# Optimization experiments

Hardware: AMD Instinct MI355X
Metric: run time of the kernel (lower is better)

The kernel has to match this reference:

```python
import jax, jax.numpy as jnp
import numpy as np

B, S, D, H, C = 2, 2048, 1024, 16, 64

def setup_inputs() -> dict:
    key = jax.random.key(0)
    kx, kq, kk, kv, ko = jax.random.split(key, 5)
    scale = 0.02
    return {
        "x": jax.random.normal(kx, (B, S, D), dtype=jnp.float32),
        "Wq": jax.random.normal(kq, (D, H, C), dtype=jnp.float32) * scale,
        "Wk": jax.random.normal(kk, (D, H, C), dtype=jnp.float32) * scale,
        "Wv": jax.random.normal(kv, (D, H, C), dtype=jnp.float32) * scale,
        "Wo": jax.random.normal(ko, (H, C, D), dtype=jnp.float32) * scale,
    }

def reference(x, Wq, Wk, Wv, Wo):
    # project to per-head q/k/v: [B,S,H,C]
    q = jnp.einsum('bqd,dhc->bqhc', x, Wq)
    k = jnp.einsum('bkd,dhc->bkhc', x, Wk)
    v = jnp.einsum('bkd,dhc->bkhc', x, Wv)
    q = q * (C ** -0.5)
    alphas = jnp.einsum('bqhc,bkhc->bhqk', q, k)  # [B,H,S,S]
    weights = jax.nn.softmax(alphas, axis=-1)
    out = jnp.einsum('bhqk,bkhc->bqhc', weights, v)
    return jnp.einsum('bqhc,hcd->bqd', out, Wo)
```

## Files before the change

kernel.cpp:

```cpp
#include <hip/hip_runtime.h>
#include <hip/hip_bf16.h>
#include <stdint.h>
#include <stddef.h>

typedef __bf16 bf16;
typedef __bf16 bf16x8 __attribute__((ext_vector_type(8)));
typedef float f32x4 __attribute__((ext_vector_type(4)));

#define DEV __device__ __forceinline__

DEV void async16(const bf16* g, bf16* l) {
    __builtin_amdgcn_global_load_lds(
        (const __attribute__((address_space(1))) void*)g,
        (__attribute__((address_space(3))) void*)l,
        16, 0, 0);
}


__global__ void convert_x(const float* __restrict__ in, bf16* __restrict__ out, int n) {
    int i = (blockIdx.x * blockDim.x + threadIdx.x) * 4;
    if (i >= n) return;
    const float4 v = *(const float4*)(in + i);
    bf16 o4[4] = {(bf16)v.x, (bf16)v.y, (bf16)v.z, (bf16)v.w};
    *(uint2*)(out + i) = *(const uint2*)o4;
}

__global__ void transpose_cvt_all(const float* __restrict__ Wq, const float* __restrict__ Wk,
                                  const float* __restrict__ Wv, const float* __restrict__ Wo,
                                  bf16* __restrict__ WqkvT, bf16* __restrict__ WoT) {
    const float* src;
    bf16* dst;
    float scale = 1.0f;
    switch (blockIdx.z) {
        case 0: src = Wq; dst = WqkvT; scale = 0.125f * 1.4426950408889634f; break;
        case 1: src = Wk; dst = WqkvT + 1024 * 1024; break;
        case 2: src = Wv; dst = WqkvT + 2 * 1024 * 1024; break;
        default: src = Wo; dst = WoT; break;
    }
    __shared__ float t[32][33];
    const int c0 = blockIdx.x * 32, r0 = blockIdx.y * 32;
    const int tx = threadIdx.x & 31, ty = threadIdx.x >> 5;
#pragma unroll
    for (int i = 0; i < 32; i += 8)
        t[ty + i][tx] = src[(size_t)(r0 + ty + i) * 1024 + c0 + tx];
    __syncthreads();
#pragma unroll
    for (int i = 0; i < 32; i += 8)
        dst[(size_t)(c0 + ty + i) * 1024 + r0 + tx] = (bf16)(t[tx][ty + i] * scale);
}

__global__ void transpose_v(const bf16* __restrict__ V, bf16* __restrict__ VT) {
    __shared__ bf16 t[32][33];
    const int c0 = blockIdx.x * 32, r0 = blockIdx.y * 32;
    const int tx = threadIdx.x & 31, ty = threadIdx.x >> 5;
#pragma unroll
    for (int i = 0; i < 32; i += 8)
        t[ty + i][tx] = V[(size_t)(r0 + ty + i) * 3072 + c0 + tx];
    __syncthreads();
#pragma unroll
    for (int i = 0; i < 32; i += 8)
        VT[(size_t)(c0 + ty + i) * 4096 + r0 + tx] = t[tx][ty + i];
}


template <bool OUT_F32>
__global__ __launch_bounds__(256, 2) void gemm_bt(
    const bf16* __restrict__ A, const bf16* __restrict__ BT, void* __restrict__ Cout,
    int M, int N, int K) {
    __shared__ __attribute__((aligned(16))) bf16 As[128 * 32];
    __shared__ __attribute__((aligned(16))) bf16 Bs[128 * 32];
    const int tid = threadIdx.x;
    const int wid = tid >> 6;
    const int lane = tid & 63;
    const int quad = lane >> 4;
    const int l16 = lane & 15;
    const int wm = wid >> 1, wn = wid & 1;
    const int m0 = blockIdx.y * 128, n0 = blockIdx.x * 128;

    const int srow = wid * 32 + (lane >> 2);
    const int skcol = (lane & 3) * 8;
    const bf16* ag = A + (size_t)(m0 + srow) * K + skcol;
    const bf16* bg = BT + (size_t)(n0 + srow) * K + skcol;
    bf16* as0 = &As[(wid * 32) * 32];
    bf16* as1 = &As[(wid * 32 + 16) * 32];
    bf16* bs0 = &Bs[(wid * 32) * 32];
    bf16* bs1 = &Bs[(wid * 32 + 16) * 32];

    f32x4 acc[4][4];
#pragma unroll
    for (int i = 0; i < 4; ++i)
#pragma unroll
        for (int j = 0; j < 4; ++j) acc[i][j] = (f32x4){0.f, 0.f, 0.f, 0.f};

    for (int k0 = 0; k0 < K; k0 += 32) {
        async16(ag + k0, as0);
        async16(ag + (size_t)16 * K + k0, as1);
        async16(bg + k0, bs0);
        async16(bg + (size_t)16 * K + k0, bs1);
        __syncthreads();

        bf16x8 af[4], bfr[4];
#pragma unroll
        for (int mi = 0; mi < 4; ++mi)
            af[mi] = *(const bf16x8*)&As[(wm * 64 + mi * 16 + l16) * 32 + quad * 8];
#pragma unroll
        for (int ni = 0; ni < 4; ++ni)
            bfr[ni] = *(const bf16x8*)&Bs[(wn * 64 + ni * 16 + l16) * 32 + quad * 8];
#pragma unroll
        for (int mi = 0; mi < 4; ++mi)
#pragma unroll
            for (int ni = 0; ni < 4; ++ni)
                acc[mi][ni] = __builtin_amdgcn_mfma_f32_16x16x32_bf16(
                    af[mi], bfr[ni], acc[mi][ni], 0, 0, 0);
        __syncthreads();
    }

    if (OUT_F32) {
        float* C = (float*)Cout;
#pragma unroll
        for (int mi = 0; mi < 4; ++mi)
#pragma unroll
            for (int ni = 0; ni < 4; ++ni)
#pragma unroll
                for (int r = 0; r < 4; ++r)
                    C[(size_t)(m0 + wm * 64 + mi * 16 + quad * 4 + r) * N +
                      (n0 + wn * 64 + ni * 16 + l16)] = acc[mi][ni][r];
    } else {
        bf16* C = (bf16*)Cout;
#pragma unroll
        for (int mi = 0; mi < 4; ++mi)
#pragma unroll
            for (int ni = 0; ni < 4; ++ni)
#pragma unroll
                for (int r = 0; r < 4; ++r)
                    C[(size_t)(m0 + wm * 64 + mi * 16 + quad * 4 + r) * N +
                      (n0 + wn * 64 + ni * 16 + l16)] = (bf16)acc[mi][ni][r];
    }
}


__global__ __launch_bounds__(256, 2) void flash_attn(
    const bf16* __restrict__ QKV, const bf16* __restrict__ VT, bf16* __restrict__ O) {
    constexpr int LDK = 72;
    constexpr int LDP = 68;
    __shared__ __attribute__((aligned(16))) bf16 Ks[64 * LDK];
    __shared__ __attribute__((aligned(16))) bf16 Vs[64 * LDK];
    __shared__ __attribute__((aligned(16))) bf16 Ps[128 * LDP];

    const int tid = threadIdx.x, wid = tid >> 6, lane = tid & 63;
    const int quad = lane >> 4, l16 = lane & 15;
    const int qt = blockIdx.x;
    const int bh = blockIdx.y;
    const int b = bh >> 4, h = bh & 15;
    const int q0 = qt * 128;

    const int row8 = tid >> 3, col8 = (tid & 7) * 8;

    {
        const bf16* qg = QKV + (size_t)(b * 2048 + q0 + row8) * 3072 + h * 64 + col8;
#pragma unroll
        for (int p = 0; p < 4; ++p)
            *(bf16x8*)&Ps[(p * 32 + row8) * LDP + col8] =
                *(const bf16x8*)(qg + (size_t)(p * 32) * 3072);
    }
    __syncthreads();
    bf16x8 qf[2][2];
#pragma unroll
    for (int mi = 0; mi < 2; ++mi)
#pragma unroll
        for (int ks = 0; ks < 2; ++ks)
            qf[mi][ks] = *(const bf16x8*)&Ps[(wid * 32 + mi * 16 + l16) * LDP + ks * 32 + quad * 8];

    const bf16* kg = QKV + (size_t)(b * 2048 + row8) * 3072 + 1024 + h * 64 + col8;
    const bf16* vg = VT + (size_t)(h * 64 + row8) * 4096 + b * 2048 + col8;

    bf16x8 kr0 = *(const bf16x8*)(kg);
    bf16x8 kr1 = *(const bf16x8*)(kg + (size_t)32 * 3072);
    bf16x8 vr0 = *(const bf16x8*)(vg);
    bf16x8 vr1 = *(const bf16x8*)(vg + (size_t)32 * 4096);

    f32x4 o[2][4];
    float lsum[2][4];
#pragma unroll
    for (int mi = 0; mi < 2; ++mi) {
#pragma unroll
        for (int ni = 0; ni < 4; ++ni) o[mi][ni] = (f32x4){0.f, 0.f, 0.f, 0.f};
#pragma unroll
        for (int r = 0; r < 4; ++r) lsum[mi][r] = 0.f;
    }

    for (int kc = 0; kc < 32; ++kc) {
        *(bf16x8*)&Ks[row8 * LDK + col8] = kr0;
        *(bf16x8*)&Ks[(row8 + 32) * LDK + col8] = kr1;
        *(bf16x8*)&Vs[row8 * LDK + col8] = vr0;
        *(bf16x8*)&Vs[(row8 + 32) * LDK + col8] = vr1;
        __syncthreads();

        if (kc < 31) {
            const size_t ko = (size_t)(kc + 1) * 64;
            kr0 = *(const bf16x8*)(kg + ko * 3072);
            kr1 = *(const bf16x8*)(kg + (ko + 32) * 3072);
            vr0 = *(const bf16x8*)(vg + ko);
            vr1 = *(const bf16x8*)(vg + (size_t)32 * 4096 + ko);
        }

        f32x4 s[2][4];
#pragma unroll
        for (int mi = 0; mi < 2; ++mi)
#pragma unroll
            for (int ni = 0; ni < 4; ++ni) s[mi][ni] = (f32x4){0.f, 0.f, 0.f, 0.f};
#pragma unroll
        for (int ni = 0; ni < 4; ++ni) {
            const bf16x8 kf0 = *(const bf16x8*)&Ks[(ni * 16 + l16) * LDK + quad * 8];
            const bf16x8 kf1 = *(const bf16x8*)&Ks[(ni * 16 + l16) * LDK + 32 + quad * 8];
#pragma unroll
            for (int mi = 0; mi < 2; ++mi) {
                s[mi][ni] = __builtin_amdgcn_mfma_f32_16x16x32_bf16(qf[mi][0], kf0, s[mi][ni], 0, 0, 0);
                s[mi][ni] = __builtin_amdgcn_mfma_f32_16x16x32_bf16(qf[mi][1], kf1, s[mi][ni], 0, 0, 0);
            }
        }

#pragma unroll
        for (int mi = 0; mi < 2; ++mi)
#pragma unroll
            for (int ni = 0; ni < 4; ++ni)
#pragma unroll
                for (int r = 0; r < 4; ++r) {
                    const float p = __builtin_amdgcn_exp2f(s[mi][ni][r]);
                    lsum[mi][r] += p;
                    Ps[(wid * 32 + mi * 16 + quad * 4 + r) * LDP + ni * 16 + l16] = (bf16)p;
                }

#pragma unroll
        for (int ks = 0; ks < 2; ++ks) {
            bf16x8 pf[2];
#pragma unroll
            for (int mi = 0; mi < 2; ++mi)
                pf[mi] = *(const bf16x8*)&Ps[(wid * 32 + mi * 16 + l16) * LDP + ks * 32 + quad * 8];
#pragma unroll
            for (int ni = 0; ni < 4; ++ni) {
                const bf16x8 vf = *(const bf16x8*)&Vs[(ni * 16 + l16) * LDK + ks * 32 + quad * 8];
#pragma unroll
                for (int mi = 0; mi < 2; ++mi)
                    o[mi][ni] = __builtin_amdgcn_mfma_f32_16x16x32_bf16(pf[mi], vf, o[mi][ni], 0, 0, 0);
            }
        }
        __syncthreads();
    }

#pragma unroll
    for (int off = 1; off < 16; off <<= 1)
#pragma unroll
        for (int mi = 0; mi < 2; ++mi)
#pragma unroll
            for (int r = 0; r < 4; ++r) lsum[mi][r] += __shfl_xor(lsum[mi][r], off);

    float inv[2][4];
#pragma unroll
    for (int mi = 0; mi < 2; ++mi)
#pragma unroll
        for (int r = 0; r < 4; ++r) inv[mi][r] = 1.0f / lsum[mi][r];

#pragma unroll
    for (int mi = 0; mi < 2; ++mi)
#pragma unroll
        for (int ni = 0; ni < 4; ++ni)
#pragma unroll
            for (int r = 0; r < 4; ++r)
                O[(size_t)(b * 2048 + q0 + wid * 32 + mi * 16 + quad * 4 + r) * 1024 +
                  (h * 64 + ni * 16 + l16)] = (bf16)(o[mi][ni][r] * inv[mi][r]);
}


extern "C" void kernel_launch(void* const* d_in, const int* in_sizes, int n_in,
                              void* d_out, int out_size, void* d_ws, size_t ws_size,
                              hipStream_t stream) {
    (void)in_sizes; (void)n_in; (void)out_size; (void)ws_size;
    const float* x  = (const float*)d_in[0];
    const float* Wq = (const float*)d_in[1];
    const float* Wk = (const float*)d_in[2];
    const float* Wv = (const float*)d_in[3];
    const float* Wo = (const float*)d_in[4];

    char* ws = (char*)d_ws;
    bf16* xb    = (bf16*)(ws);
    bf16* att   = xb;
    bf16* WqkvT = (bf16*)(ws + (size_t)8  * 1024 * 1024);
    bf16* WoT   = (bf16*)(ws + (size_t)14 * 1024 * 1024);
    bf16* QKV   = (bf16*)(ws + (size_t)16 * 1024 * 1024);
    bf16* VT    = (bf16*)(ws + (size_t)40 * 1024 * 1024);

    const int n_x = 2 * 2048 * 1024;
    convert_x<<<n_x / (256 * 4), 256, 0, stream>>>(x, xb, n_x);

    transpose_cvt_all<<<dim3(32, 32, 4), 256, 0, stream>>>(Wq, Wk, Wv, Wo, WqkvT, WoT);

    gemm_bt<false><<<dim3(3072 / 128, 4096 / 128), 256, 0, stream>>>(
        xb, WqkvT, QKV, 4096, 3072, 1024);

    transpose_v<<<dim3(32, 128), 256, 0, stream>>>(QKV + 2048, VT);

    flash_attn<<<dim3(16, 32), 256, 0, stream>>>(QKV, VT, att);

    gemm_bt<true><<<dim3(1024 / 128, 4096 / 128), 256, 0, stream>>>(
        att, WoT, (float*)d_out, 4096, 1024, 1024);
}
```

Measured before the change: 204.5 us.

## Split attention over key halves with combine kernel; deepen GEMM K step

The attention grid is split into two halves along the key dimension, doubling the block count from 512. Each block writes unnormalized fp32 partial outputs and row sums, and a new combine_att kernel adds the two halves, normalizes, and converts to bf16. This relies on the softmax having no running-max rescaling, since partials are simply summed. Separately, the projection GEMM now loads 64 K-elements per barrier pair instead of 32 and raises its occupancy hint. The trade-off is an extra 32 MB of fp32 partial traffic, one more kernel launch, and more shared memory per GEMM block.

Measured after the change: 205.0 us. Within noise of the previous version (+0.2%).

```diff
diff --git a/kernel.cpp b/kernel.cpp
--- a/kernel.cpp
+++ b/kernel.cpp
@@ -64,11 +64,11 @@
 
 
 template <bool OUT_F32>
-__global__ __launch_bounds__(256, 2) void gemm_bt(
+__global__ __launch_bounds__(256, 3) void gemm_bt(
     const bf16* __restrict__ A, const bf16* __restrict__ BT, void* __restrict__ Cout,
     int M, int N, int K) {
-    __shared__ __attribute__((aligned(16))) bf16 As[128 * 32];
-    __shared__ __attribute__((aligned(16))) bf16 Bs[128 * 32];
+    __shared__ __attribute__((aligned(16))) bf16 As[2 * 128 * 32];
+    __shared__ __attribute__((aligned(16))) bf16 Bs[2 * 128 * 32];
     const int tid = threadIdx.x;
     const int wid = tid >> 6;
     const int lane = tid & 63;
@@ -81,10 +81,6 @@
     const int skcol = (lane & 3) * 8;
     const bf16* ag = A + (size_t)(m0 + srow) * K + skcol;
     const bf16* bg = BT + (size_t)(n0 + srow) * K + skcol;
-    bf16* as0 = &As[(wid * 32) * 32];
-    bf16* as1 = &As[(wid * 32 + 16) * 32];
-    bf16* bs0 = &Bs[(wid * 32) * 32];
-    bf16* bs1 = &Bs[(wid * 32 + 16) * 32];
 
     f32x4 acc[4][4];
 #pragma unroll
@@ -92,26 +88,32 @@
 #pragma unroll
         for (int j = 0; j < 4; ++j) acc[i][j] = (f32x4){0.f, 0.f, 0.f, 0.f};
 
-    for (int k0 = 0; k0 < K; k0 += 32) {
-        async16(ag + k0, as0);
-        async16(ag + (size_t)16 * K + k0, as1);
-        async16(bg + k0, bs0);
-        async16(bg + (size_t)16 * K + k0, bs1);
+    for (int k0 = 0; k0 < K; k0 += 64) {
+#pragma unroll
+        for (int p = 0; p < 2; ++p) {
+            async16(ag + k0 + p * 32, &As[p * 4096 + (wid * 32) * 32]);
+            async16(ag + (size_t)16 * K + k0 + p * 32, &As[p * 4096 + (wid * 32 + 16) * 32]);
+            async16(bg + k0 + p * 32, &Bs[p * 4096 + (wid * 32) * 32]);
+            async16(bg + (size_t)16 * K + k0 + p * 32, &Bs[p * 4096 + (wid * 32 + 16) * 32]);
+        }
         __syncthreads();
 
-        bf16x8 af[4], bfr[4];
-#pragma unroll
-        for (int mi = 0; mi < 4; ++mi)
-            af[mi] = *(const bf16x8*)&As[(wm * 64 + mi * 16 + l16) * 32 + quad * 8];
-#pragma unroll
-        for (int ni = 0; ni < 4; ++ni)
-            bfr[ni] = *(const bf16x8*)&Bs[(wn * 64 + ni * 16 + l16) * 32 + quad * 8];
-#pragma unroll
-        for (int mi = 0; mi < 4; ++mi)
+#pragma unroll
+        for (int ks = 0; ks < 2; ++ks) {
+            bf16x8 af[4], bfr[4];
+#pragma unroll
+            for (int mi = 0; mi < 4; ++mi)
+                af[mi] = *(const bf16x8*)&As[ks * 4096 + (wm * 64 + mi * 16 + l16) * 32 + quad * 8];
 #pragma unroll
             for (int ni = 0; ni < 4; ++ni)
-                acc[mi][ni] = __builtin_amdgcn_mfma_f32_16x16x32_bf16(
-                    af[mi], bfr[ni], acc[mi][ni], 0, 0, 0);
+                bfr[ni] = *(const bf16x8*)&Bs[ks * 4096 + (wn * 64 + ni * 16 + l16) * 32 + quad * 8];
+#pragma unroll
+            for (int mi = 0; mi < 4; ++mi)
+#pragma unroll
+                for (int ni = 0; ni < 4; ++ni)
+                    acc[mi][ni] = __builtin_amdgcn_mfma_f32_16x16x32_bf16(
+                        af[mi], bfr[ni], acc[mi][ni], 0, 0, 0);
+        }
         __syncthreads();
     }
 
@@ -139,8 +141,9 @@
 }
 
 
-__global__ __launch_bounds__(256, 2) void flash_attn(
-    const bf16* __restrict__ QKV, const bf16* __restrict__ VT, bf16* __restrict__ O) {
+__global__ __launch_bounds__(256, 4) void flash_attn(
+    const bf16* __restrict__ QKV, const bf16* __restrict__ VT,
+    float* __restrict__ op, float* __restrict__ lp) {
     constexpr int LDK = 72;
     constexpr int LDP = 68;
     __shared__ __attribute__((aligned(16))) bf16 Ks[64 * LDK];
@@ -151,6 +154,7 @@
     const int quad = lane >> 4, l16 = lane & 15;
     const int qt = blockIdx.x;
     const int bh = blockIdx.y;
+    const int kh = blockIdx.z;
     const int b = bh >> 4, h = bh & 15;
     const int q0 = qt * 128;
 
@@ -171,8 +175,8 @@
         for (int ks = 0; ks < 2; ++ks)
             qf[mi][ks] = *(const bf16x8*)&Ps[(wid * 32 + mi * 16 + l16) * LDP + ks * 32 + quad * 8];
 
-    const bf16* kg = QKV + (size_t)(b * 2048 + row8) * 3072 + 1024 + h * 64 + col8;
-    const bf16* vg = VT + (size_t)(h * 64 + row8) * 4096 + b * 2048 + col8;
+    const bf16* kg = QKV + (size_t)(b * 2048 + kh * 1024 + row8) * 3072 + 1024 + h * 64 + col8;
+    const bf16* vg = VT + (size_t)(h * 64 + row8) * 4096 + b * 2048 + kh * 1024 + col8;
 
     bf16x8 kr0 = *(const bf16x8*)(kg);
     bf16x8 kr1 = *(const bf16x8*)(kg + (size_t)32 * 3072);
@@ -189,14 +193,14 @@
         for (int r = 0; r < 4; ++r) lsum[mi][r] = 0.f;
     }
 
-    for (int kc = 0; kc < 32; ++kc) {
+    for (int kc = 0; kc < 16; ++kc) {
         *(bf16x8*)&Ks[row8 * LDK + col8] = kr0;
         *(bf16x8*)&Ks[(row8 + 32) * LDK + col8] = kr1;
         *(bf16x8*)&Vs[row8 * LDK + col8] = vr0;
         *(bf16x8*)&Vs[(row8 + 32) * LDK + col8] = vr1;
         __syncthreads();
 
-        if (kc < 31) {
+        if (kc < 15) {
             const size_t ko = (size_t)(kc + 1) * 64;
             kr0 = *(const bf16x8*)(kg + ko * 3072);
             kr1 = *(const bf16x8*)(kg + (ko + 32) * 3072);
@@ -255,20 +259,36 @@
 #pragma unroll
             for (int r = 0; r < 4; ++r) lsum[mi][r] += __shfl_xor(lsum[mi][r], off);
 
-    float inv[2][4];
+    if (l16 == 0) {
+#pragma unroll
+        for (int mi = 0; mi < 2; ++mi)
+#pragma unroll
+            for (int r = 0; r < 4; ++r)
+                lp[(size_t)kh * 4096 * 16 +
+                   (size_t)(b * 2048 + q0 + wid * 32 + mi * 16 + quad * 4 + r) * 16 + h] = lsum[mi][r];
+    }
 #pragma unroll
     for (int mi = 0; mi < 2; ++mi)
 #pragma unroll
-        for (int r = 0; r < 4; ++r) inv[mi][r] = 1.0f / lsum[mi][r];
-
-#pragma unroll
-    for (int mi = 0; mi < 2; ++mi)
-#pragma unroll
         for (int ni = 0; ni < 4; ++ni)
 #pragma unroll
             for (int r = 0; r < 4; ++r)
-                O[(size_t)(b * 2048 + q0 + wid * 32 + mi * 16 + quad * 4 + r) * 1024 +
-                  (h * 64 + ni * 16 + l16)] = (bf16)(o[mi][ni][r] * inv[mi][r]);
+                op[(size_t)kh * 4096 * 1024 +
+                   (size_t)(b * 2048 + q0 + wid * 32 + mi * 16 + quad * 4 + r) * 1024 +
+                   (h * 64 + ni * 16 + l16)] = o[mi][ni][r];
+}
+
+__global__ void combine_att(const float* __restrict__ op, const float* __restrict__ lp,
+                            bf16* __restrict__ att) {
+    const int idx = (blockIdx.x * 256 + threadIdx.x) * 4;
+    const int q = idx >> 10, h = (idx & 1023) >> 6;
+    const float4 a = *(const float4*)(op + idx);
+    const float4 c = *(const float4*)(op + (size_t)4096 * 1024 + idx);
+    const float l = lp[q * 16 + h] + lp[4096 * 16 + q * 16 + h];
+    const float inv = 1.0f / l;
+    bf16 r[4] = {(bf16)((a.x + c.x) * inv), (bf16)((a.y + c.y) * inv),
+                 (bf16)((a.z + c.z) * inv), (bf16)((a.w + c.w) * inv)};
+    *(uint2*)(att + idx) = *(const uint2*)r;
 }
 
 
@@ -289,6 +309,8 @@
     bf16* WoT   = (bf16*)(ws + (size_t)14 * 1024 * 1024);
     bf16* QKV   = (bf16*)(ws + (size_t)16 * 1024 * 1024);
     bf16* VT    = (bf16*)(ws + (size_t)40 * 1024 * 1024);
+    float* op   = (float*)(ws + (size_t)48 * 1024 * 1024);
+    float* lp   = (float*)(ws + (size_t)80 * 1024 * 1024);
 
     const int n_x = 2 * 2048 * 1024;
     convert_x<<<n_x / (256 * 4), 256, 0, stream>>>(x, xb, n_x);
@@ -300,7 +322,9 @@
 
     transpose_v<<<dim3(32, 128), 256, 0, stream>>>(QKV + 2048, VT);
 
-    flash_attn<<<dim3(16, 32), 256, 0, stream>>>(QKV, VT, att);
+    flash_attn<<<dim3(16, 32, 2), 256, 0, stream>>>(QKV, VT, op, lp);
+
+    combine_att<<<4096, 256, 0, stream>>>(op, lp, att);
 
     gemm_bt<true><<<dim3(1024 / 128, 4096 / 128), 256, 0, stream>>>(
         att, WoT, (float*)d_out, 4096, 1024, 1024);
```
